# Kernel optimization log

Measured on AMD Instinct MI355X. Metric: run time of the kernel, lower is better.

## Reference

```python
import jax, jax.numpy as jnp
import numpy as np

EMB = 768
HEADS = 3
HD = EMB // HEADS  # 256
B, S = 4, 2048


def setup_inputs() -> dict:
    key = jax.random.key(0)
    ks = jax.random.split(key, 8)
    inputs_for_keys = jax.random.normal(ks[0], (B, S, EMB), dtype=jnp.float32)
    inputs_for_values = jax.random.normal(ks[1], (B, S, EMB), dtype=jnp.float32)
    inputs_for_queries = jax.random.normal(ks[2], (B, S, EMB), dtype=jnp.float32)
    # stacked per-head projection weights: [heads, emb, head_dim]
    # original uses 'random_uniform' init (small uniform); scale ~0.05
    Wk = jax.random.uniform(ks[3], (HEADS, EMB, HD), jnp.float32, -0.05, 0.05)
    Wv = jax.random.uniform(ks[4], (HEADS, EMB, HD), jnp.float32, -0.05, 0.05)
    Wq = jax.random.uniform(ks[5], (HEADS, EMB, HD), jnp.float32, -0.05, 0.05)
    Wo = jax.random.normal(ks[6], (EMB, EMB), dtype=jnp.float32) * (1.0 / np.sqrt(EMB))
    bo = jnp.zeros((EMB,), dtype=jnp.float32)
    return {
        "inputs_for_keys": inputs_for_keys,
        "inputs_for_values": inputs_for_values,
        "inputs_for_queries": inputs_for_queries,
        "Wk": Wk, "Wv": Wv, "Wq": Wq, "Wo": Wo, "bo": bo,
    }


def reference(inputs_for_keys, inputs_for_values, inputs_for_queries, Wk, Wv, Wq, Wo, bo):
    # per-head projections, batched over heads: [b, h, s, f]
    K = jnp.einsum('bse,hef->bhsf', inputs_for_keys, Wk)
    V = jnp.einsum('bse,hef->bhsf', inputs_for_values, Wv)
    Q = jnp.einsum('bse,hef->bhsf', inputs_for_queries, Wq)

    seq_k = inputs_for_keys.shape[1]
    seq_q = inputs_for_queries.shape[1]
    # NOTE: original scales by sqrt(window_size_keys) (seq len), not sqrt(d_k)
    scale = jnp.sqrt(jnp.float32(seq_k))

    scores = jnp.einsum('bhqf,bhkf->bhqk', Q, K) / scale
    # causal mask: -inf strictly above the diagonal (j > i)
    mask = jnp.triu(jnp.full((seq_q, seq_k), -jnp.inf, dtype=scores.dtype), k=1)
    scores = scores + mask

    attn = jax.nn.softmax(scores, axis=-1)  # [b,h,q,k]
    heads = jnp.einsum('bhqk,bhkf->bhqf', attn, V)

    # concat heads along feature dim: [b, q, heads*hd]
    b, h, q, f = heads.shape
    concat = heads.transpose(0, 2, 1, 3).reshape(b, q, h * f)
    return concat @ Wo + bo
```

## Files before the change

### kernel.cpp

```cpp
#include <hip/hip_runtime.h>

#define BATCH 4
#define NHEADS 3
#define SEQ 2048
#define HDIM 256
#define EMBD 768
#define MTOT (BATCH*SEQ)
#define WSZ (NHEADS*EMBD*HDIM)

typedef unsigned short u16x8 __attribute__((ext_vector_type(8)));
typedef unsigned short u16x4 __attribute__((ext_vector_type(4)));
typedef __bf16 bf16x8 __attribute__((ext_vector_type(8)));
typedef float fx4 __attribute__((ext_vector_type(4)));

__device__ __forceinline__ unsigned short f2bf(float x) {
    union { float f; unsigned int u; } v; v.f = x;
    unsigned int r = v.u + 0x7fffu + ((v.u >> 16) & 1u);
    return (unsigned short)(r >> 16);
}

__device__ __forceinline__ fx4 mfma16(u16x8 a, u16x8 b, fx4 c) {
    return __builtin_amdgcn_mfma_f32_16x16x32_bf16(
        __builtin_bit_cast(bf16x8, a), __builtin_bit_cast(bf16x8, b), c, 0, 0, 0);
}

__device__ __forceinline__ void gl_lds16(const unsigned short* g, unsigned short* l) {
    __builtin_amdgcn_global_load_lds(
        (const __attribute__((address_space(1))) unsigned int*)g,
        (__attribute__((address_space(3))) unsigned int*)l, 16, 0, 0);
}

__device__ const unsigned char attn_sched[48] = {
    124,125, 63, 120,121, 116,117, 59, 112,113, 108,109, 55, 104,105,
    100,101, 51,  96, 97,  92, 93, 47,  88, 89,  84, 85, 43,  80, 81,
     76, 77, 39,  72, 73,  68, 69, 35,  64, 65,  31, 27, 23, 19, 15,
     11,  7,  3
};

__global__ __launch_bounds__(256) void castAw_kernel(
    const float* __restrict__ Ak, const float* __restrict__ Av,
    const float* __restrict__ Aq,
    const float* __restrict__ Wk, const float* __restrict__ Wv,
    const float* __restrict__ Wq, const float* __restrict__ Wo,
    unsigned short* __restrict__ Abf, unsigned short* __restrict__ Wt,
    unsigned short* __restrict__ Wot)
{
    __shared__ float tile[64][65];
    int bx = blockIdx.x;
    if (bx < 9216) {
        int e = (bx * 256 + threadIdx.x) * 8;
        int t = e / (MTOT * EMBD);
        int r = e - t * (MTOT * EMBD);
        const float* A = (t == 0) ? Ak : (t == 1) ? Av : Aq;
        const fx4* s = (const fx4*)(A + r);
        fx4 v0 = s[0], v1 = s[1];
        u16x8 o;
        o[0]=f2bf(v0[0]); o[1]=f2bf(v0[1]); o[2]=f2bf(v0[2]); o[3]=f2bf(v0[3]);
        o[4]=f2bf(v1[0]); o[5]=f2bf(v1[1]); o[6]=f2bf(v1[2]); o[7]=f2bf(v1[3]);
        *(u16x8*)(Abf + e) = o;
        return;
    }
    int z = bx - 9216;
    const float* src; unsigned short* dst;
    int src_ld, dst_ld, e0, f0;
    if (z < 432) {
        int t = z / 144, rem = z - t * 144;
        int h = rem / 48, tl = rem - h * 48;
        e0 = (tl % 12) * 64; f0 = (tl / 12) * 64;
        const float* W = (t == 0) ? Wk : (t == 1) ? Wv : Wq;
        src = W + h * 768 * 256; src_ld = 256;
        dst = Wt + t * WSZ + h * 256 * 768; dst_ld = 768;
    } else {
        int zz = z - 432;
        e0 = (zz % 12) * 64; f0 = (zz / 12) * 64;
        src = Wo; src_ld = 768;
        dst = Wot; dst_ld = 768;
    }
    int tx = threadIdx.x & 63, ty4 = threadIdx.x >> 6;
    #pragma unroll
    for (int i = 0; i < 16; ++i) {
        int r = ty4 + i * 4;
        tile[r][tx] = src[(e0 + r) * src_ld + f0 + tx];
    }
    __syncthreads();
    #pragma unroll
    for (int i = 0; i < 16; ++i) {
        int r = ty4 + i * 4;
        dst[(f0 + r) * dst_ld + e0 + tx] = f2bf(tile[tx][r]);
    }
}

__global__ __launch_bounds__(256) void proj_kernel(
    const unsigned short* __restrict__ Abf, const unsigned short* __restrict__ Wt,
    unsigned short* __restrict__ Kg, unsigned short* __restrict__ Vg,
    unsigned short* __restrict__ Qg)
{
    __shared__ alignas(16) unsigned short S[17408];
    unsigned short* As = S;
    unsigned short* Bs = S + 8192;

    int z = blockIdx.z;
    const unsigned short* A = Abf + z * (MTOT * EMBD);
    int m0 = blockIdx.x * 128;
    int h = blockIdx.y >> 1, fbase = (blockIdx.y & 1) * 128;
    const unsigned short* W = Wt + z * WSZ + (h * 256 + fbase) * EMBD;

    int tid = threadIdx.x;
    int w = tid >> 6, ln = tid & 63;
    int lane16 = ln & 15, quad = ln >> 4;
    int mw = (w & 1) * 64, nw = (w >> 1) * 64;

    fx4 acc[4][4];
    #pragma unroll
    for (int i = 0; i < 4; ++i)
        #pragma unroll
        for (int j = 0; j < 4; ++j) acc[i][j] = (fx4){0.f, 0.f, 0.f, 0.f};

    int c0 = tid, c1 = tid + 256;
    int r0 = c0 >> 2, s0_ = ((c0 & 3) ^ ((c0 >> 3) & 3)) * 8;
    int r1 = c1 >> 2, s1_ = ((c1 & 3) ^ ((c1 >> 3) & 3)) * 8;
    const unsigned short* Ag0 = A + (m0 + r0) * EMBD + s0_;
    const unsigned short* Ag1 = A + (m0 + r1) * EMBD + s1_;
    const unsigned short* Wg0 = W + r0 * EMBD + s0_;
    const unsigned short* Wg1 = W + r1 * EMBD + s1_;

    int fsw = (quad ^ ((lane16 >> 1) & 3)) * 8;

    for (int kb = 0; kb < EMBD; kb += 32) {
        __syncthreads();
        gl_lds16(Ag0 + kb, &As[c0 * 8]);
        gl_lds16(Ag1 + kb, &As[c1 * 8]);
        gl_lds16(Wg0 + kb, &Bs[c0 * 8]);
        gl_lds16(Wg1 + kb, &Bs[c1 * 8]);
        __syncthreads();

        u16x8 af[4], bf[4];
        #pragma unroll
        for (int i = 0; i < 4; ++i) {
            af[i] = *(const u16x8*)&As[(mw + i * 16 + lane16) * 32 + fsw];
            bf[i] = *(const u16x8*)&Bs[(nw + i * 16 + lane16) * 32 + fsw];
        }
        #pragma unroll
        for (int i = 0; i < 4; ++i)
            #pragma unroll
            for (int j = 0; j < 4; ++j)
                acc[i][j] = mfma16(af[i], bf[j], acc[i][j]);
    }

    __syncthreads();
    int b = m0 >> 11, sq0 = m0 & 2047;

    if (z == 1) {
        #pragma unroll
        for (int i = 0; i < 4; ++i)
            #pragma unroll
            for (int j = 0; j < 4; ++j) {
                int fl = nw + j * 16 + lane16;
                int ml = mw + i * 16 + quad * 4;
                u16x4 pk;
                pk[0] = f2bf(acc[i][j][0]); pk[1] = f2bf(acc[i][j][1]);
                pk[2] = f2bf(acc[i][j][2]); pk[3] = f2bf(acc[i][j][3]);
                *(u16x4*)&S[fl * 136 + ml] = pk;
            }
        __syncthreads();
        int fl = tid >> 1, mseg = (tid & 1) * 64;
        const unsigned short* srcp = &S[fl * 136 + mseg];
        unsigned short* dstp = Vg + ((b * NHEADS + h) * HDIM + fbase + fl) * SEQ + sq0 + mseg;
        #pragma unroll
        for (int c = 0; c < 8; ++c)
            *(u16x8*)(dstp + c * 8) = *(const u16x8*)(srcp + c * 8);
    } else {
        #pragma unroll
        for (int i = 0; i < 4; ++i)
            #pragma unroll
            for (int j = 0; j < 4; ++j) {
                int fl = nw + j * 16 + lane16;
                int ml = mw + i * 16 + quad * 4;
                #pragma unroll
                for (int r = 0; r < 4; ++r)
                    S[(ml + r) * 136 + fl] = f2bf(acc[i][j][r]);
            }
        __syncthreads();
        unsigned short* dst0 = (z == 0) ? Kg : Qg;
        int ml = tid >> 1, fseg = (tid & 1) * 64;
        const unsigned short* srcp = &S[ml * 136 + fseg];
        unsigned short* dstp = dst0 + ((b * NHEADS + h) * SEQ + sq0 + ml) * HDIM + fbase + fseg;
        #pragma unroll
        for (int c = 0; c < 8; ++c)
            *(u16x8*)(dstp + c * 8) = *(const u16x8*)(srcp + c * 8);
    }
}

__global__ __launch_bounds__(256) void attn_kernel(
    const unsigned short* __restrict__ Kg, const unsigned short* __restrict__ Vg,
    const unsigned short* __restrict__ Qg, unsigned short* __restrict__ heads,
    float* __restrict__ Opart, float* __restrict__ Lpart)
{
    __shared__ alignas(16) unsigned short Ks[64 * 256];
    __shared__ alignas(16) unsigned short Vs[256 * 64];

    int bx = blockIdx.x;
    int bh = bx % 12;
    int ent = attn_sched[bx / 12];
    int qt = ent >> 2, kc = ent & 3;
    int tid = threadIdx.x;
    int w = tid >> 6, ln = tid & 63;
    int lane16 = ln & 15, quad = ln >> 4;
    int q0w = qt * 64 + w * 16;

    const unsigned short* Kbase = Kg + bh * (SEQ * HDIM);
    const unsigned short* Vbase = Vg + bh * (SEQ * HDIM);
    const unsigned short* Qbase = Qg + bh * (SEQ * HDIM);

    u16x8 qf[8];
    {
        const unsigned short* qrow = Qbase + (q0w + lane16) * HDIM + quad * 8;
        #pragma unroll
        for (int c = 0; c < 8; ++c) qf[c] = *(const u16x8*)(qrow + c * 32);
    }

    fx4 o[16];
    #pragma unroll
    for (int i = 0; i < 16; ++i) o[i] = (fx4){0.f, 0.f, 0.f, 0.f};
    float lsum = 0.f;

    const float Cs2 = 0.03188010519640429f;

    int t0, t1;
    if (kc == 3) { t0 = 0; t1 = qt + 1; }
    else         { int half = (qt + 1) >> 1;
                   t0 = kc ? half : 0; t1 = kc ? qt + 1 : half; }

    const unsigned short* kgp = Kbase + (tid >> 5) * HDIM
                              + (((tid & 31) ^ (tid >> 5)) * 8);
    const unsigned short* vgp = Vbase + (tid >> 3) * SEQ
                              + (((tid & 7) ^ ((tid >> 3) & 7)) * 8);
    unsigned short* ksl = &Ks[tid * 8];
    unsigned short* vsl = &Vs[tid * 8];

    int ksw = lane16 & 7;

    for (int kt = t0; kt < t1; ++kt) {
        int k0 = kt * 64;
        __syncthreads();
        #pragma unroll
        for (int j = 0; j < 8; ++j)
            gl_lds16(kgp + (k0 + j * 8) * HDIM, ksl + j * 2048);
        #pragma unroll
        for (int j = 0; j < 8; ++j)
            gl_lds16(vgp + j * 32 * SEQ + k0, vsl + j * 2048);
        __syncthreads();

        fx4 sacc[4];
        #pragma unroll
        for (int ks = 0; ks < 4; ++ks) sacc[ks] = (fx4){0.f,0.f,0.f,0.f};
        #pragma unroll
        for (int c = 0; c < 8; ++c) {
            #pragma unroll
            for (int ks = 0; ks < 4; ++ks) {
                u16x8 kf = *(const u16x8*)&Ks[(ks * 16 + lane16) * 256
                                              + (((c * 4 + quad) ^ ksw) << 3)];
                sacc[ks] = mfma16(kf, qf[c], sacc[ks]);
            }
        }

        float p[4][4];
        int q = q0w + lane16;
        #pragma unroll
        for (int ks = 0; ks < 4; ++ks)
            #pragma unroll
            for (int r = 0; r < 4; ++r) {
                int ka_ = k0 + ks * 16 + quad * 4 + r;
                float e = exp2f(sacc[ks][r] * Cs2);
                p[ks][r] = (ka_ <= q) ? e : 0.f;
                lsum += p[ks][r];
            }

        #pragma unroll
        for (int hh = 0; hh < 2; ++hh) {
            u16x8 pf;
            #pragma unroll
            for (int j = 0; j < 8; ++j) {
                int srcLane = ((((quad << 1) + (j >> 2)) & 3) << 4) | lane16;
                float v0 = __shfl(p[2 * hh][j & 3], srcLane, 64);
                float v1 = __shfl(p[2 * hh + 1][j & 3], srcLane, 64);
                pf[j] = f2bf(quad >= 2 ? v1 : v0);
            }
            #pragma unroll
            for (int ft = 0; ft < 16; ++ft) {
                u16x8 vf = *(const u16x8*)&Vs[(ft * 16 + lane16) * 64
                                              + (((hh * 4 + quad) ^ ksw) << 3)];
                o[ft] = mfma16(pf, vf, o[ft]);
            }
        }
    }

    lsum += __shfl_xor(lsum, 16, 64);
    lsum += __shfl_xor(lsum, 32, 64);

    if (kc == 3) {
        float linv = 1.f / lsum;
        float inv[4];
        #pragma unroll
        for (int r = 0; r < 4; ++r) inv[r] = __shfl(linv, quad * 4 + r, 64);
        int b = bh / 3, h = bh - (bh / 3) * 3;
        unsigned short* hp = heads + (b * SEQ + q0w + quad * 4) * EMBD + h * HDIM + lane16;
        #pragma unroll
        for (int ft = 0; ft < 16; ++ft)
            #pragma unroll
            for (int r = 0; r < 4; ++r)
                hp[r * EMBD + ft * 16] = f2bf(o[ft][r] * inv[r]);
    } else {
        int slot = (bh * 16 + (qt - 16)) * 2 + kc;
        float* Op = Opart + slot * 16384 + (w * 16 + quad * 4) * 256 + lane16;
        #pragma unroll
        for (int ft = 0; ft < 16; ++ft)
            #pragma unroll
            for (int r = 0; r < 4; ++r)
                Op[r * 256 + ft * 16] = o[ft][r];
        if (quad == 0) Lpart[slot * 64 + w * 16 + lane16] = lsum;
    }
}

__global__ __launch_bounds__(256) void combine_kernel(
    const float* __restrict__ Opart, const float* __restrict__ Lpart,
    unsigned short* __restrict__ heads)
{
    int t = blockIdx.x;
    int bh = t >> 4, qt = (t & 15) + 16;
    int s0 = t * 2, s1 = s0 + 1;
    int tid = threadIdx.x;
    int row = tid >> 2, fseg = (tid & 3) * 64;
    float l = Lpart[s0 * 64 + row] + Lpart[s1 * 64 + row];
    float inv = 1.f / l;
    const fx4* O0 = (const fx4*)(Opart + s0 * 16384 + row * 256 + fseg);
    const fx4* O1 = (const fx4*)(Opart + s1 * 16384 + row * 256 + fseg);
    int b = bh / 3, h = bh - (bh / 3) * 3;
    unsigned short* hp = heads + (b * SEQ + qt * 64 + row) * EMBD + h * HDIM + fseg;
    #pragma unroll
    for (int i = 0; i < 16; ++i) {
        fx4 v = O0[i] + O1[i];
        u16x4 pk;
        pk[0] = f2bf(v[0] * inv); pk[1] = f2bf(v[1] * inv);
        pk[2] = f2bf(v[2] * inv); pk[3] = f2bf(v[3] * inv);
        *(u16x4*)(hp + i * 4) = pk;
    }
}

__global__ __launch_bounds__(256) void outproj_kernel(
    const unsigned short* __restrict__ A, const unsigned short* __restrict__ Wot,
    const float* __restrict__ bo, float* __restrict__ out)
{
    __shared__ alignas(16) unsigned short S[16384];
    unsigned short* As = S;
    unsigned short* Bs = S + 8192;

    int m0 = blockIdx.x * 128, n0 = blockIdx.y * 128;
    int tid = threadIdx.x;
    int w = tid >> 6, ln = tid & 63;
    int lane16 = ln & 15, quad = ln >> 4;
    int mw = (w & 1) * 64, nw = (w >> 1) * 64;

    fx4 acc[4][4];
    #pragma unroll
    for (int i = 0; i < 4; ++i)
        #pragma unroll
        for (int j = 0; j < 4; ++j) acc[i][j] = (fx4){0.f, 0.f, 0.f, 0.f};

    int c0 = tid, c1 = tid + 256;
    int r0 = c0 >> 2, s0_ = ((c0 & 3) ^ ((c0 >> 3) & 3)) * 8;
    int r1 = c1 >> 2, s1_ = ((c1 & 3) ^ ((c1 >> 3) & 3)) * 8;
    const unsigned short* Ag0 = A + (m0 + r0) * EMBD + s0_;
    const unsigned short* Ag1 = A + (m0 + r1) * EMBD + s1_;
    const unsigned short* Wg0 = Wot + (n0 + r0) * EMBD + s0_;
    const unsigned short* Wg1 = Wot + (n0 + r1) * EMBD + s1_;

    int fsw = (quad ^ ((lane16 >> 1) & 3)) * 8;

    for (int kb = 0; kb < EMBD; kb += 32) {
        __syncthreads();
        gl_lds16(Ag0 + kb, &As[c0 * 8]);
        gl_lds16(Ag1 + kb, &As[c1 * 8]);
        gl_lds16(Wg0 + kb, &Bs[c0 * 8]);
        gl_lds16(Wg1 + kb, &Bs[c1 * 8]);
        __syncthreads();

        u16x8 af[4], bf[4];
        #pragma unroll
        for (int i = 0; i < 4; ++i) {
            af[i] = *(const u16x8*)&As[(mw + i * 16 + lane16) * 32 + fsw];
            bf[i] = *(const u16x8*)&Bs[(nw + i * 16 + lane16) * 32 + fsw];
        }
        #pragma unroll
        for (int i = 0; i < 4; ++i)
            #pragma unroll
            for (int j = 0; j < 4; ++j)
                acc[i][j] = mfma16(af[i], bf[j], acc[i][j]);
    }

    #pragma unroll
    for (int i = 0; i < 4; ++i) {
        int mb = m0 + mw + i * 16 + quad * 4;
        #pragma unroll
        for (int j = 0; j < 4; ++j) {
            int n = n0 + nw + j * 16 + lane16;
            float bias = bo[n];
            #pragma unroll
            for (int r = 0; r < 4; ++r)
                out[(mb + r) * EMBD + n] = acc[i][j][r] + bias;
        }
    }
}

extern "C" void kernel_launch(void* const* d_in, const int* in_sizes, int n_in,
                              void* d_out, int out_size, void* d_ws, size_t ws_size,
                              hipStream_t stream) {
    const float* Ak = (const float*)d_in[0];
    const float* Av = (const float*)d_in[1];
    const float* Aq = (const float*)d_in[2];
    const float* Wk = (const float*)d_in[3];
    const float* Wv = (const float*)d_in[4];
    const float* Wq = (const float*)d_in[5];
    const float* Wo = (const float*)d_in[6];
    const float* bo = (const float*)d_in[7];
    float* out = (float*)d_out;

    char* base = (char*)d_ws;
    unsigned short* Wt    = (unsigned short*)(base);
    unsigned short* Wot   = (unsigned short*)(base + 3538944);
    unsigned short* Abf   = (unsigned short*)(base + 4718592);
    unsigned short* Kg    = (unsigned short*)(base + 42467328);
    unsigned short* Vg    = (unsigned short*)(base + 55050240);
    unsigned short* Qg    = (unsigned short*)(base + 67633152);
    unsigned short* heads = (unsigned short*)(base + 80216064);
    float* Opart = (float*)(base + 4718592);
    float* Lpart = (float*)(base + 4718592 + 25165824);

    castAw_kernel<<<dim3(9792), dim3(256), 0, stream>>>(
        Ak, Av, Aq, Wk, Wv, Wq, Wo, Abf, Wt, Wot);
    proj_kernel<<<dim3(64, 6, 3), dim3(256), 0, stream>>>(
        Abf, Wt, Kg, Vg, Qg);
    attn_kernel<<<dim3(576), dim3(256), 0, stream>>>(
        Kg, Vg, Qg, heads, Opart, Lpart);
    combine_kernel<<<dim3(192), dim3(256), 0, stream>>>(Opart, Lpart, heads);
    outproj_kernel<<<dim3(64, 6), dim3(256), 0, stream>>>(heads, Wot, bo, out);
}
```

Before: 312.8 us.

## Restructure projection GEMMs: stream A from registers, stage weight half-K panels in LDS

Both the QKV projection and output projection GEMMs now use 256x64 tiles. Each wave loads its A rows directly from global memory into registers, with a one-step register prefetch. The 64-row weight panel is staged in LDS for half of K at a time with an XOR swizzle, which cuts per-k-step barriers from 24 to 2. This removes the A tile's LDS traffic and most synchronisation, but relies on uncoalesced 16-byte global A loads and the cache for reuse, and it raises register pressure (launch_bounds 256,3).

```diff
diff --git a/kernel.cpp b/kernel.cpp
--- a/kernel.cpp
+++ b/kernel.cpp
@@ -90,25 +90,24 @@
     }
 }
 
-__global__ __launch_bounds__(256) void proj_kernel(
+__global__ __launch_bounds__(256, 3) void proj_kernel(
     const unsigned short* __restrict__ Abf, const unsigned short* __restrict__ Wt,
     unsigned short* __restrict__ Kg, unsigned short* __restrict__ Vg,
     unsigned short* __restrict__ Qg)
 {
-    __shared__ alignas(16) unsigned short S[17408];
-    unsigned short* As = S;
-    unsigned short* Bs = S + 8192;
+    __shared__ alignas(16) unsigned short Bs[24576];
 
     int z = blockIdx.z;
     const unsigned short* A = Abf + z * (MTOT * EMBD);
-    int m0 = blockIdx.x * 128;
-    int h = blockIdx.y >> 1, fbase = (blockIdx.y & 1) * 128;
+    int m0 = blockIdx.x * 256;
+    int nb = blockIdx.y;
+    int h = nb >> 2, fbase = (nb & 3) * 64;
     const unsigned short* W = Wt + z * WSZ + (h * 256 + fbase) * EMBD;
 
     int tid = threadIdx.x;
     int w = tid >> 6, ln = tid & 63;
     int lane16 = ln & 15, quad = ln >> 4;
-    int mw = (w & 1) * 64, nw = (w >> 1) * 64;
+    int mw = w * 64;
 
     fx4 acc[4][4];
     #pragma unroll
@@ -116,78 +115,98 @@
         #pragma unroll
         for (int j = 0; j < 4; ++j) acc[i][j] = (fx4){0.f, 0.f, 0.f, 0.f};
 
-    int c0 = tid, c1 = tid + 256;
-    int r0 = c0 >> 2, s0_ = ((c0 & 3) ^ ((c0 >> 3) & 3)) * 8;
-    int r1 = c1 >> 2, s1_ = ((c1 & 3) ^ ((c1 >> 3) & 3)) * 8;
-    const unsigned short* Ag0 = A + (m0 + r0) * EMBD + s0_;
-    const unsigned short* Ag1 = A + (m0 + r1) * EMBD + s1_;
-    const unsigned short* Wg0 = W + r0 * EMBD + s0_;
-    const unsigned short* Wg1 = W + r1 * EMBD + s1_;
-
-    int fsw = (quad ^ ((lane16 >> 1) & 3)) * 8;
-
-    for (int kb = 0; kb < EMBD; kb += 32) {
-        __syncthreads();
-        gl_lds16(Ag0 + kb, &As[c0 * 8]);
-        gl_lds16(Ag1 + kb, &As[c1 * 8]);
-        gl_lds16(Wg0 + kb, &Bs[c0 * 8]);
-        gl_lds16(Wg1 + kb, &Bs[c1 * 8]);
-        __syncthreads();
-
-        u16x8 af[4], bf[4];
-        #pragma unroll
-        for (int i = 0; i < 4; ++i) {
-            af[i] = *(const u16x8*)&As[(mw + i * 16 + lane16) * 32 + fsw];
-            bf[i] = *(const u16x8*)&Bs[(nw + i * 16 + lane16) * 32 + fsw];
-        }
+    const unsigned short* Ap = A + (m0 + mw + lane16) * EMBD + quad * 8;
+
+    u16x8 afc[4], afn[4];
+    #pragma unroll
+    for (int i = 0; i < 4; ++i) afc[i] = *(const u16x8*)(Ap + i * 16 * EMBD);
+
+    int bsw = lane16 & 7;
+
+    #pragma unroll
+    for (int ph = 0; ph < 2; ++ph) {
+        __syncthreads();
+        #pragma unroll
+        for (int jj = 0; jj < 12; ++jj) {
+            int U = jj * 256 + tid;
+            int row = U / 48;
+            int slot = U - row * 48;
+            int gu = (slot & ~7) | ((slot & 7) ^ (row & 7));
+            gl_lds16(W + row * EMBD + ph * 384 + gu * 8, &Bs[U * 8]);
+        }
+        __syncthreads();
+
+        #pragma unroll
+        for (int kk = 0; kk < 12; ++kk) {
+            int kbn = ph * 384 + kk * 32 + 32;
+            if (kbn < EMBD) {
+                #pragma unroll
+                for (int i = 0; i < 4; ++i)
+                    afn[i] = *(const u16x8*)(Ap + i * 16 * EMBD + kbn);
+            }
+            #pragma unroll
+            for (int j = 0; j < 4; ++j) {
+                int u = kk * 4 + quad;
+                int slot = (u & ~7) | ((u & 7) ^ bsw);
+                u16x8 bf = *(const u16x8*)&Bs[((j * 16 + lane16) * 48 + slot) * 8];
+                #pragma unroll
+                for (int i = 0; i < 4; ++i)
+                    acc[i][j] = mfma16(afc[i], bf, acc[i][j]);
+            }
+            if (kbn < EMBD) {
+                #pragma unroll
+                for (int i = 0; i < 4; ++i) afc[i] = afn[i];
+            }
+        }
+    }
+
+    int b = m0 >> 11, sq0 = m0 & 2047;
+
+    if (z == 1) {
+        __syncthreads();
         #pragma unroll
         for (int i = 0; i < 4; ++i)
             #pragma unroll
-            for (int j = 0; j < 4; ++j)
-                acc[i][j] = mfma16(af[i], bf[j], acc[i][j]);
-    }
-
-    __syncthreads();
-    int b = m0 >> 11, sq0 = m0 & 2047;
-
-    if (z == 1) {
-        #pragma unroll
-        for (int i = 0; i < 4; ++i)
-            #pragma unroll
             for (int j = 0; j < 4; ++j) {
-                int fl = nw + j * 16 + lane16;
+                int fl = j * 16 + lane16;
                 int ml = mw + i * 16 + quad * 4;
                 u16x4 pk;
                 pk[0] = f2bf(acc[i][j][0]); pk[1] = f2bf(acc[i][j][1]);
                 pk[2] = f2bf(acc[i][j][2]); pk[3] = f2bf(acc[i][j][3]);
-                *(u16x4*)&S[fl * 136 + ml] = pk;
-            }
-        __syncthreads();
-        int fl = tid >> 1, mseg = (tid & 1) * 64;
-        const unsigned short* srcp = &S[fl * 136 + mseg];
-        unsigned short* dstp = Vg + ((b * NHEADS + h) * HDIM + fbase + fl) * SEQ + sq0 + mseg;
+                *(u16x4*)&Bs[fl * 264 + ml] = pk;
+            }
+        __syncthreads();
+        int fl = tid >> 2, seg = (tid & 3) * 64;
+        const unsigned short* sp = &Bs[fl * 264 + seg];
+        unsigned short* dp = Vg + ((size_t)(b * NHEADS + h) * HDIM + fbase + fl) * SEQ
+                           + sq0 + seg;
         #pragma unroll
         for (int c = 0; c < 8; ++c)
-            *(u16x8*)(dstp + c * 8) = *(const u16x8*)(srcp + c * 8);
+            *(u16x8*)(dp + c * 8) = *(const u16x8*)(sp + c * 8);
     } else {
-        #pragma unroll
-        for (int i = 0; i < 4; ++i)
-            #pragma unroll
-            for (int j = 0; j < 4; ++j) {
-                int fl = nw + j * 16 + lane16;
-                int ml = mw + i * 16 + quad * 4;
-                #pragma unroll
-                for (int r = 0; r < 4; ++r)
-                    S[(ml + r) * 136 + fl] = f2bf(acc[i][j][r]);
-            }
-        __syncthreads();
         unsigned short* dst0 = (z == 0) ? Kg : Qg;
-        int ml = tid >> 1, fseg = (tid & 1) * 64;
-        const unsigned short* srcp = &S[ml * 136 + fseg];
-        unsigned short* dstp = dst0 + ((b * NHEADS + h) * SEQ + sq0 + ml) * HDIM + fbase + fseg;
-        #pragma unroll
-        for (int c = 0; c < 8; ++c)
-            *(u16x8*)(dstp + c * 8) = *(const u16x8*)(srcp + c * 8);
+        #pragma unroll
+        for (int q = 0; q < 2; ++q) {
+            __syncthreads();
+            #pragma unroll
+            for (int i = 0; i < 4; ++i)
+                #pragma unroll
+                for (int j2 = 0; j2 < 2; ++j2) {
+                    int jj = q * 2 + j2;
+                    int row = mw + i * 16 + quad * 4;
+                    int col = j2 * 16 + lane16;
+                    #pragma unroll
+                    for (int r = 0; r < 4; ++r)
+                        Bs[(row + r) * 40 + col] = f2bf(acc[i][jj][r]);
+                }
+            __syncthreads();
+            const unsigned short* sp = &Bs[tid * 40];
+            unsigned short* dp = dst0 + ((size_t)(b * NHEADS + h) * SEQ + sq0 + tid) * HDIM
+                               + fbase + q * 32;
+            #pragma unroll
+            for (int c = 0; c < 4; ++c)
+                *(u16x8*)(dp + c * 8) = *(const u16x8*)(sp + c * 8);
+        }
     }
 }
 
@@ -347,19 +366,20 @@
     }
 }
 
-__global__ __launch_bounds__(256) void outproj_kernel(
+__global__ __launch_bounds__(256, 3) void outproj_kernel(
     const unsigned short* __restrict__ A, const unsigned short* __restrict__ Wot,
     const float* __restrict__ bo, float* __restrict__ out)
 {
-    __shared__ alignas(16) unsigned short S[16384];
-    unsigned short* As = S;
-    unsigned short* Bs = S + 8192;
-
-    int m0 = blockIdx.x * 128, n0 = blockIdx.y * 128;
+    __shared__ alignas(16) unsigned short Bs[24576];
+
+    int m0 = blockIdx.x * 256;
+    int nb = blockIdx.y;
+    const unsigned short* W = Wot + (nb * 64) * EMBD;
+
     int tid = threadIdx.x;
     int w = tid >> 6, ln = tid & 63;
     int lane16 = ln & 15, quad = ln >> 4;
-    int mw = (w & 1) * 64, nw = (w >> 1) * 64;
+    int mw = w * 64;
 
     fx4 acc[4][4];
     #pragma unroll
@@ -367,47 +387,61 @@
         #pragma unroll
         for (int j = 0; j < 4; ++j) acc[i][j] = (fx4){0.f, 0.f, 0.f, 0.f};
 
-    int c0 = tid, c1 = tid + 256;
-    int r0 = c0 >> 2, s0_ = ((c0 & 3) ^ ((c0 >> 3) & 3)) * 8;
-    int r1 = c1 >> 2, s1_ = ((c1 & 3) ^ ((c1 >> 3) & 3)) * 8;
-    const unsigned short* Ag0 = A + (m0 + r0) * EMBD + s0_;
-    const unsigned short* Ag1 = A + (m0 + r1) * EMBD + s1_;
-    const unsigned short* Wg0 = Wot + (n0 + r0) * EMBD + s0_;
-    const unsigned short* Wg1 = Wot + (n0 + r1) * EMBD + s1_;
-
-    int fsw = (quad ^ ((lane16 >> 1) & 3)) * 8;
-
-    for (int kb = 0; kb < EMBD; kb += 32) {
-        __syncthreads();
-        gl_lds16(Ag0 + kb, &As[c0 * 8]);
-        gl_lds16(Ag1 + kb, &As[c1 * 8]);
-        gl_lds16(Wg0 + kb, &Bs[c0 * 8]);
-        gl_lds16(Wg1 + kb, &Bs[c1 * 8]);
-        __syncthreads();
-
-        u16x8 af[4], bf[4];
+    const unsigned short* Ap = A + (m0 + mw + lane16) * EMBD + quad * 8;
+
+    u16x8 afc[4], afn[4];
+    #pragma unroll
+    for (int i = 0; i < 4; ++i) afc[i] = *(const u16x8*)(Ap + i * 16 * EMBD);
+
+    int bsw = lane16 & 7;
+
+    #pragma unroll
+    for (int ph = 0; ph < 2; ++ph) {
+        __syncthreads();
+        #pragma unroll
+        for (int jj = 0; jj < 12; ++jj) {
+            int U = jj * 256 + tid;
+            int row = U / 48;
+            int slot = U - row * 48;
+            int gu = (slot & ~7) | ((slot & 7) ^ (row & 7));
+            gl_lds16(W + row * EMBD + ph * 384 + gu * 8, &Bs[U * 8]);
+        }
+        __syncthreads();
+
+        #pragma unroll
+        for (int kk = 0; kk < 12; ++kk) {
+            int kbn = ph * 384 + kk * 32 + 32;
+            if (kbn < EMBD) {
+                #pragma unroll
+                for (int i = 0; i < 4; ++i)
+                    afn[i] = *(const u16x8*)(Ap + i * 16 * EMBD + kbn);
+            }
+            #pragma unroll
+            for (int j = 0; j < 4; ++j) {
+                int u = kk * 4 + quad;
+                int slot = (u & ~7) | ((u & 7) ^ bsw);
+                u16x8 bf = *(const u16x8*)&Bs[((j * 16 + lane16) * 48 + slot) * 8];
+                #pragma unroll
+                for (int i = 0; i < 4; ++i)
+                    acc[i][j] = mfma16(afc[i], bf, acc[i][j]);
+            }
+            if (kbn < EMBD) {
+                #pragma unroll
+                for (int i = 0; i < 4; ++i) afc[i] = afn[i];
+            }
+        }
+    }
+
+    #pragma unroll
+    for (int j = 0; j < 4; ++j) {
+        int n = nb * 64 + j * 16 + lane16;
+        float bias = bo[n];
         #pragma unroll
         for (int i = 0; i < 4; ++i) {
-            af[i] = *(const u16x8*)&As[(mw + i * 16 + lane16) * 32 + fsw];
-            bf[i] = *(const u16x8*)&Bs[(nw + i * 16 + lane16) * 32 + fsw];
-        }
-        #pragma unroll
-        for (int i = 0; i < 4; ++i)
-            #pragma unroll
-            for (int j = 0; j < 4; ++j)
-                acc[i][j] = mfma16(af[i], bf[j], acc[i][j]);
-    }
-
-    #pragma unroll
-    for (int i = 0; i < 4; ++i) {
-        int mb = m0 + mw + i * 16 + quad * 4;
-        #pragma unroll
-        for (int j = 0; j < 4; ++j) {
-            int n = n0 + nw + j * 16 + lane16;
-            float bias = bo[n];
+            int mb = m0 + mw + i * 16 + quad * 4;
             #pragma unroll
             for (int r = 0; r < 4; ++r)
-                out[(mb + r) * EMBD + n] = acc[i][j][r] + bias;
+                out[(size_t)(mb + r) * EMBD + n] = acc[i][j][r] + bias;
         }
     }
 }
@@ -438,10 +472,10 @@
 
     castAw_kernel<<<dim3(9792), dim3(256), 0, stream>>>(
         Ak, Av, Aq, Wk, Wv, Wq, Wo, Abf, Wt, Wot);
-    proj_kernel<<<dim3(64, 6, 3), dim3(256), 0, stream>>>(
+    proj_kernel<<<dim3(32, 12, 3), dim3(256), 0, stream>>>(
         Abf, Wt, Kg, Vg, Qg);
     attn_kernel<<<dim3(576), dim3(256), 0, stream>>>(
         Kg, Vg, Qg, heads, Opart, Lpart);
     combine_kernel<<<dim3(192), dim3(256), 0, stream>>>(Opart, Lpart, heads);
-    outproj_kernel<<<dim3(64, 6), dim3(256), 0, stream>>>(heads, Wot, bo, out);
-}
+    outproj_kernel<<<dim3(32, 12), dim3(256), 0, stream>>>(heads, Wot, bo, out);
+}
```

After: 307.1 us. About the same (-1.8%).
